# Kernel tuning notes

Measured on AMD Instinct MI355X. Metric: run time of the kernel, lower is better.

The kernel has to match this reference:

```python
import jax, jax.numpy as jnp
import numpy as np

DIM = 768
HEADS = 8
HEAD_DIM = DIM // HEADS
SCALE = DIM ** (-0.5)  # faithful: original scales by dimension**-0.5, not head_dim


def setup_inputs() -> dict:
    key = jax.random.key(0)
    k1, k2, k3 = jax.random.split(key, 3)
    B, N = 2, 4096
    x = jax.random.normal(k1, (B, N, DIM), dtype=jnp.float32)
    # qkv projection params (Linear(dim, 3*dim))
    W_qkv = jax.random.normal(k2, (DIM, 3 * DIM), dtype=jnp.float32) * (DIM ** -0.5)
    b_qkv = jax.random.normal(k3, (3 * DIM,), dtype=jnp.float32) * 0.01
    return {"x": x, "W_qkv": W_qkv, "b_qkv": b_qkv}


def reference(x, W_qkv, b_qkv):
    B, N, D = x.shape
    qkv = x @ W_qkv + b_qkv                       # (B, N, 3D)
    qkv = qkv.reshape(B, N, 3, HEADS, HEAD_DIM)
    q, k, v = jnp.moveaxis(qkv, 2, 0)             # each (B, N, H, dh)
    # (B, H, N, N) scores — explicit materialization as in the source
    scores = jnp.einsum('bnhd,bmhd->bhnm', q, k) * SCALE
    attn = jax.nn.softmax(scores, axis=-1)
    out = jnp.einsum('bhnm,bmhd->bnhd', attn, v)  # (B, N, H, dh)
    return out.reshape(B, N, D)
```

## Files before the change

### kernel.cpp

```cpp
#include <hip/hip_runtime.h>
#include <hip/hip_bf16.h>


typedef __attribute__((ext_vector_type(8)))  short    bf16x8;
typedef __attribute__((ext_vector_type(4)))  float    floatx4;
typedef __attribute__((ext_vector_type(16))) float    floatx16;
typedef __attribute__((ext_vector_type(8)))  unsigned short us8;
typedef __attribute__((ext_vector_type(4)))  unsigned short us4;

#define HEADS 8
#define DH 96
#define NSEQ 4096
#define DIM 768
#define SCALE2_F (0.03608439182435161f * 1.4426950408889634f)

__device__ __forceinline__ unsigned short f2bf(float f) {
    union { float f; unsigned u; } v; v.f = f;
    unsigned r = v.u + 0x7fffu + ((v.u >> 16) & 1u);
    return (unsigned short)(r >> 16);
}

__device__ __forceinline__ unsigned pk2(float a, float b) {
    float2 t; t.x = a; t.y = b;
    __hip_bfloat162 r = __float22bfloat162_rn(t);
    return *(unsigned*)&r;
}

__device__ __forceinline__ bf16x8 mk_pfrag(float c0, float c1, float c2, float c3,
                                           float c4, float c5, float c6, float c7, int hB) {
    unsigned pl0 = pk2(c0, c1), pl1 = pk2(c2, c3);
    unsigned pu0 = pk2(c4, c5), pu1 = pk2(c6, c7);
    unsigned s0 = hB ? pl0 : pu0, s1 = hB ? pl1 : pu1;
    unsigned r0 = (unsigned)__shfl_xor((int)s0, 32);
    unsigned r1 = (unsigned)__shfl_xor((int)s1, 32);
    union { unsigned u[4]; bf16x8 v; } f;
    f.u[0] = hB ? r0 : pl0;
    f.u[1] = hB ? r1 : pl1;
    f.u[2] = hB ? pu0 : r0;
    f.u[3] = hB ? pu1 : r1;
    return f.v;
}

__global__ __launch_bounds__(256) void cvt_x(const float* __restrict__ x, unsigned short* __restrict__ xb) {
    int i = blockIdx.x * 256 + threadIdx.x;
    float4 v = ((const float4*)x)[i];
    us4 o; o.x = f2bf(v.x); o.y = f2bf(v.y); o.z = f2bf(v.z); o.w = f2bf(v.w);
    ((us4*)xb)[i] = o;
}

__global__ __launch_bounds__(256) void cvt_w(const float* __restrict__ w, unsigned short* __restrict__ wt) {
    __shared__ unsigned short sm[64][33];
    int c0 = blockIdx.x * 32, k0 = blockIdx.y * 64;
    int t = threadIdx.x;
    int cl = t & 31, kl0 = t >> 5;
    for (int i = 0; i < 8; ++i) {
        int kl = kl0 + i * 8;
        sm[kl][cl] = f2bf(w[(k0 + kl) * 2304 + c0 + cl]);
    }
    __syncthreads();
    int kl2 = t & 63, cl0 = t >> 6;
    for (int i = 0; i < 8; ++i) {
        int cl2 = cl0 + i * 4;
        wt[(c0 + cl2) * 768 + k0 + kl2] = sm[kl2][cl2];
    }
}

__global__ __launch_bounds__(256) void gemm_qkv(const unsigned short* __restrict__ xb,
                                                const unsigned short* __restrict__ wt,
                                                const float* __restrict__ bias,
                                                unsigned short* __restrict__ qb,
                                                unsigned short* __restrict__ kb,
                                                unsigned short* __restrict__ vt) {
    __shared__ unsigned short As[128 * 72];
    __shared__ unsigned short Bs[128 * 72];
    const int tid = threadIdx.x;
    const int lane = tid & 63, wv = tid >> 6;
    const int n15 = lane & 15, quad = lane >> 4;
    const int m0 = blockIdx.y * 128, c0 = blockIdx.x * 128;
    const int mw = (wv >> 1) * 64, nw = (wv & 1) * 64;
    floatx4 acc[4][4] = {};

    for (int kt = 0; kt < 12; ++kt) {
        for (int i = 0; i < 4; ++i) {
            int g = i * 256 + tid;
            int row = g >> 3, gc = g & 7;
            *(us8*)&As[row * 72 + gc * 8] = *(const us8*)&xb[(m0 + row) * 768 + kt * 64 + gc * 8];
            *(us8*)&Bs[row * 72 + gc * 8] = *(const us8*)&wt[(c0 + row) * 768 + kt * 64 + gc * 8];
        }
        __syncthreads();
        for (int ks = 0; ks < 2; ++ks) {
            bf16x8 af[4], bfr[4];
            for (int mt = 0; mt < 4; ++mt)
                af[mt] = *(const bf16x8*)&As[(mw + mt * 16 + n15) * 72 + ks * 32 + quad * 8];
            for (int nt = 0; nt < 4; ++nt)
                bfr[nt] = *(const bf16x8*)&Bs[(nw + nt * 16 + n15) * 72 + ks * 32 + quad * 8];
            for (int mt = 0; mt < 4; ++mt)
                for (int nt = 0; nt < 4; ++nt)
                    acc[mt][nt] = __builtin_amdgcn_mfma_f32_16x16x32_bf16(af[mt], bfr[nt], acc[mt][nt], 0, 0, 0);
        }
        __syncthreads();
    }
    for (int nt = 0; nt < 4; ++nt) {
        int c = c0 + nw + nt * 16 + n15;
        float bv = bias[c];
        int which = c / 768, rem = c % 768;
        int h = rem / 96, d = rem % 96;
        for (int mt = 0; mt < 4; ++mt) {
            for (int r = 0; r < 4; ++r) {
                int m = m0 + mw + mt * 16 + quad * 4 + r;
                int b = m >> 12, n = m & 4095;
                float val = acc[mt][nt][r] + bv;
                int bh = b * HEADS + h;
                if (which == 0)      qb[(bh * NSEQ + n) * DH + d] = f2bf(val * SCALE2_F);
                else if (which == 1) kb[(bh * NSEQ + n) * DH + d] = f2bf(val);
                else                 vt[(bh * DH + d) * NSEQ + n] = f2bf(val);
            }
        }
    }
}

__global__ __launch_bounds__(128, 1) void flash(const unsigned short* __restrict__ qb,
                                                const unsigned short* __restrict__ kb,
                                                const unsigned short* __restrict__ vt,
                                                float* __restrict__ out) {
    __shared__ unsigned short sm[28672];
    __shared__ float l_all[128];

    const int tid = threadIdx.x;
    const int lane = tid & 63, wv = tid >> 6;
    const int l31 = lane & 31, h = lane >> 5;
    const int x7 = l31 & 7;
    const int id = blockIdx.x;
    const int bh = id & 15;
    const int q0 = (id >> 4) * 128 + wv * 64;

    const unsigned short* kgb = kb + (size_t)bh * NSEQ * DH;
    const unsigned short* vgb = vt + (size_t)bh * DH * NSEQ;

    bf16x8 qf[2][6];
#pragma unroll
    for (int qt = 0; qt < 2; ++qt) {
        const unsigned short* qrow = qb + (size_t)(bh * NSEQ + q0 + qt * 32 + l31) * DH;
#pragma unroll
        for (int ks = 0; ks < 6; ++ks)
            qf[qt][ks] = *(const bf16x8*)&qrow[ks * 16 + h * 8];
    }

    int kofs[2][6];
#pragma unroll
    for (int kt = 0; kt < 2; ++kt)
#pragma unroll
        for (int ks = 0; ks < 6; ++ks) {
            int b = 2 * ks + h;
            int bs = (b < 8) ? (b ^ x7) : (8 + ((b - 8) ^ x7));
            kofs[kt][ks] = (kt * 32 + l31) * 128 + bs * 8;
        }
    int vofs[3][4];
#pragma unroll
    for (int dt = 0; dt < 3; ++dt)
#pragma unroll
        for (int s = 0; s < 4; ++s)
            vofs[dt][s] = (dt * 32 + l31) * 64 + ((2 * s + h) ^ x7) * 8;

    int goffk[6], goffv[6], wofk[6], wofv[6];
#pragma unroll
    for (int i = 0; i < 6; ++i) {
        int tb = i * 128 + tid;
        int r = tb / 12, bb = tb % 12;
        goffk[i] = r * 96 + bb * 8;
        int bs = (bb < 8) ? (bb ^ (r & 7)) : (8 + ((bb - 8) ^ (r & 7)));
        wofk[i] = r * 128 + bs * 8;
        int d = tb >> 3, b2 = tb & 7;
        goffv[i] = d * 4096 + b2 * 8;
        wofv[i] = d * 64 + ((b2 ^ (d & 7))) * 8;
    }

    us8 kr[6], vr[6];
    const unsigned short* kpf = kgb;
    const unsigned short* vpf = vgb;
#pragma unroll
    for (int i = 0; i < 6; ++i) { kr[i] = *(const us8*)&kpf[goffk[i]]; vr[i] = *(const us8*)&vpf[goffv[i]]; }
    kpf += 6144; vpf += 64;
#pragma unroll
    for (int i = 0; i < 6; ++i) { *(us8*)&sm[wofk[i]] = kr[i]; *(us8*)&sm[16384 + wofv[i]] = vr[i]; }
#pragma unroll
    for (int i = 0; i < 6; ++i) { kr[i] = *(const us8*)&kpf[goffk[i]]; vr[i] = *(const us8*)&vpf[goffv[i]]; }
    kpf += 6144; vpf += 64;
    __syncthreads();

    floatx16 stA[2][2] = {}, stB[2][2] = {};
#pragma unroll
    for (int ks = 0; ks < 6; ++ks)
#pragma unroll
        for (int kt = 0; kt < 2; ++kt) {
            bf16x8 ak = *(const bf16x8*)&sm[kofs[kt][ks]];
            stA[kt][0] = __builtin_amdgcn_mfma_f32_32x32x16_bf16(ak, qf[0][ks], stA[kt][0], 0, 0, 0);
            stA[kt][1] = __builtin_amdgcn_mfma_f32_32x32x16_bf16(ak, qf[1][ks], stA[kt][1], 0, 0, 0);
        }

    floatx16 o[2][3] = {};
    float lsum[2] = {0.f, 0.f};

    auto body = [&](int kv, floatx16 (&cur)[2][2], floatx16 (&nxt)[2][2]) {
        const int nb = (kv + 1) & 1, cb = kv & 1;
        if (kv < 63) {
            unsigned short* Kd = sm + nb * 8192;
            unsigned short* Vd = sm + 16384 + nb * 6144;
#pragma unroll
            for (int i = 0; i < 6; ++i) { *(us8*)&Kd[wofk[i]] = kr[i]; *(us8*)&Vd[wofv[i]] = vr[i]; }
            if (kv < 62) {
#pragma unroll
                for (int i = 0; i < 6; ++i) { kr[i] = *(const us8*)&kpf[goffk[i]]; vr[i] = *(const us8*)&vpf[goffv[i]]; }
                kpf += 6144; vpf += 64;
            }
        }
        __syncthreads();

        const unsigned short* Kn = sm + nb * 8192;
        const unsigned short* Vc = sm + 16384 + cb * 6144;

        if (kv < 63) {
#pragma unroll
            for (int ks = 0; ks < 6; ++ks)
#pragma unroll
                for (int kt = 0; kt < 2; ++kt) {
                    bf16x8 ak = *(const bf16x8*)&Kn[kofs[kt][ks]];
                    nxt[kt][0] = __builtin_amdgcn_mfma_f32_32x32x16_bf16(ak, qf[0][ks], nxt[kt][0], 0, 0, 0);
                    nxt[kt][1] = __builtin_amdgcn_mfma_f32_32x32x16_bf16(ak, qf[1][ks], nxt[kt][1], 0, 0, 0);
                }
        }

#pragma unroll
        for (int kt = 0; kt < 2; ++kt)
#pragma unroll
            for (int qt = 0; qt < 2; ++qt)
#pragma unroll
                for (int rg = 0; rg < 16; ++rg) {
                    float p = __builtin_amdgcn_exp2f(cur[kt][qt][rg]);
                    cur[kt][qt][rg] = p;
                    lsum[qt] += p;
                }
        bf16x8 pf[2][4];
#pragma unroll
        for (int qt = 0; qt < 2; ++qt) {
            pf[qt][0] = mk_pfrag(cur[0][qt][0], cur[0][qt][1], cur[0][qt][2], cur[0][qt][3],
                                 cur[0][qt][4], cur[0][qt][5], cur[0][qt][6], cur[0][qt][7], h);
            pf[qt][1] = mk_pfrag(cur[0][qt][8], cur[0][qt][9], cur[0][qt][10], cur[0][qt][11],
                                 cur[0][qt][12], cur[0][qt][13], cur[0][qt][14], cur[0][qt][15], h);
            pf[qt][2] = mk_pfrag(cur[1][qt][0], cur[1][qt][1], cur[1][qt][2], cur[1][qt][3],
                                 cur[1][qt][4], cur[1][qt][5], cur[1][qt][6], cur[1][qt][7], h);
            pf[qt][3] = mk_pfrag(cur[1][qt][8], cur[1][qt][9], cur[1][qt][10], cur[1][qt][11],
                                 cur[1][qt][12], cur[1][qt][13], cur[1][qt][14], cur[1][qt][15], h);
        }
#pragma unroll
        for (int kt = 0; kt < 2; ++kt)
#pragma unroll
            for (int qt = 0; qt < 2; ++qt)
                cur[kt][qt] = (floatx16)(0.f);

#pragma unroll
        for (int s = 0; s < 4; ++s)
#pragma unroll
            for (int dt = 0; dt < 3; ++dt) {
                bf16x8 bv = *(const bf16x8*)&Vc[vofs[dt][s]];
                o[0][dt] = __builtin_amdgcn_mfma_f32_32x32x16_bf16(pf[0][s], bv, o[0][dt], 0, 0, 0);
                o[1][dt] = __builtin_amdgcn_mfma_f32_32x32x16_bf16(pf[1][s], bv, o[1][dt], 0, 0, 0);
            }

        __syncthreads();
    };

    for (int kv = 0; kv < 64; kv += 2) {
        body(kv, stA, stB);
        body(kv + 1, stB, stA);
    }

#pragma unroll
    for (int qt = 0; qt < 2; ++qt) {
        lsum[qt] += __shfl_xor(lsum[qt], 32);
        if (h == 0) l_all[wv * 64 + qt * 32 + l31] = lsum[qt];
    }
    __syncthreads();

    const int b = bh >> 3, hd = bh & 7;
#pragma unroll
    for (int qt = 0; qt < 2; ++qt)
#pragma unroll
        for (int rg = 0; rg < 16; ++rg) {
            int row = (rg & 3) + 8 * (rg >> 2) + 4 * h;
            float inv = 1.0f / l_all[wv * 64 + qt * 32 + row];
            int q = q0 + qt * 32 + row;
            float* op = out + (size_t)(b * NSEQ + q) * DIM + hd * DH;
#pragma unroll
            for (int dt = 0; dt < 3; ++dt)
                op[dt * 32 + l31] = o[qt][dt][rg] * inv;
        }
}

extern "C" void kernel_launch(void* const* d_in, const int* in_sizes, int n_in,
                              void* d_out, int out_size, void* d_ws, size_t ws_size,
                              hipStream_t stream) {
    const float* x    = (const float*)d_in[0];
    const float* W    = (const float*)d_in[1];
    const float* bias = (const float*)d_in[2];
    float* out = (float*)d_out;

    char* ws = (char*)d_ws;
    unsigned short* xb = (unsigned short*)(ws);
    unsigned short* wt = (unsigned short*)(ws + 12582912);
    unsigned short* qb = (unsigned short*)(ws + 16121856);
    unsigned short* kb = (unsigned short*)(ws + 28704768);
    unsigned short* vt = (unsigned short*)(ws + 41287680);

    cvt_x<<<6144, 256, 0, stream>>>(x, xb);
    cvt_w<<<dim3(72, 12), 256, 0, stream>>>(W, wt);
    gemm_qkv<<<dim3(18, 64), 256, 0, stream>>>(xb, wt, bias, qb, kb, vt);
    flash<<<512, 128, 0, stream>>>(qb, kb, vt, out);
}
```

Baseline: 279.4 us.

## Use four waves per flash block with 32 query rows each

The flash kernel now runs 256 threads per block, and each wave owns 32 query rows instead of 64. The block still covers 128 queries, so K/V tiles in shared memory are shared by four waves and each thread loads half as many K/V chunks. This cuts per-thread register use (accumulators, Q fragments, prefetch buffers) so launch bounds can request two blocks per CU, aiming for more latency hiding. In exchange each K tile fragment read from LDS feeds fewer MFMAs, which raises LDS traffic per unit of compute.

```diff
diff --git a/kernel.cpp b/kernel.cpp
--- a/kernel.cpp
+++ b/kernel.cpp
@@ -119,7 +119,7 @@
     }
 }
 
-__global__ __launch_bounds__(128, 1) void flash(const unsigned short* __restrict__ qb,
+__global__ __launch_bounds__(256, 2) void flash(const unsigned short* __restrict__ qb,
                                                 const unsigned short* __restrict__ kb,
                                                 const unsigned short* __restrict__ vt,
                                                 float* __restrict__ out) {
@@ -132,18 +132,17 @@
     const int x7 = l31 & 7;
     const int id = blockIdx.x;
     const int bh = id & 15;
-    const int q0 = (id >> 4) * 128 + wv * 64;
+    const int q0 = (id >> 4) * 128 + wv * 32;
 
     const unsigned short* kgb = kb + (size_t)bh * NSEQ * DH;
     const unsigned short* vgb = vt + (size_t)bh * DH * NSEQ;
 
-    bf16x8 qf[2][6];
-#pragma unroll
-    for (int qt = 0; qt < 2; ++qt) {
-        const unsigned short* qrow = qb + (size_t)(bh * NSEQ + q0 + qt * 32 + l31) * DH;
+    bf16x8 qf[6];
+    {
+        const unsigned short* qrow = qb + (size_t)(bh * NSEQ + q0 + l31) * DH;
 #pragma unroll
         for (int ks = 0; ks < 6; ++ks)
-            qf[qt][ks] = *(const bf16x8*)&qrow[ks * 16 + h * 8];
+            qf[ks] = *(const bf16x8*)&qrow[ks * 16 + h * 8];
     }
 
     int kofs[2][6];
@@ -162,10 +161,10 @@
         for (int s = 0; s < 4; ++s)
             vofs[dt][s] = (dt * 32 + l31) * 64 + ((2 * s + h) ^ x7) * 8;
 
-    int goffk[6], goffv[6], wofk[6], wofv[6];
-#pragma unroll
-    for (int i = 0; i < 6; ++i) {
-        int tb = i * 128 + tid;
+    int goffk[3], goffv[3], wofk[3], wofv[3];
+#pragma unroll
+    for (int i = 0; i < 3; ++i) {
+        int tb = i * 256 + tid;
         int r = tb / 12, bb = tb % 12;
         goffk[i] = r * 96 + bb * 8;
         int bs = (bb < 8) ? (bb ^ (r & 7)) : (8 + ((bb - 8) ^ (r & 7)));
@@ -175,42 +174,41 @@
         wofv[i] = d * 64 + ((b2 ^ (d & 7))) * 8;
     }
 
-    us8 kr[6], vr[6];
+    us8 kr[3], vr[3];
     const unsigned short* kpf = kgb;
     const unsigned short* vpf = vgb;
 #pragma unroll
-    for (int i = 0; i < 6; ++i) { kr[i] = *(const us8*)&kpf[goffk[i]]; vr[i] = *(const us8*)&vpf[goffv[i]]; }
+    for (int i = 0; i < 3; ++i) { kr[i] = *(const us8*)&kpf[goffk[i]]; vr[i] = *(const us8*)&vpf[goffv[i]]; }
     kpf += 6144; vpf += 64;
 #pragma unroll
-    for (int i = 0; i < 6; ++i) { *(us8*)&sm[wofk[i]] = kr[i]; *(us8*)&sm[16384 + wofv[i]] = vr[i]; }
-#pragma unroll
-    for (int i = 0; i < 6; ++i) { kr[i] = *(const us8*)&kpf[goffk[i]]; vr[i] = *(const us8*)&vpf[goffv[i]]; }
+    for (int i = 0; i < 3; ++i) { *(us8*)&sm[wofk[i]] = kr[i]; *(us8*)&sm[16384 + wofv[i]] = vr[i]; }
+#pragma unroll
+    for (int i = 0; i < 3; ++i) { kr[i] = *(const us8*)&kpf[goffk[i]]; vr[i] = *(const us8*)&vpf[goffv[i]]; }
     kpf += 6144; vpf += 64;
     __syncthreads();
 
-    floatx16 stA[2][2] = {}, stB[2][2] = {};
+    floatx16 stA[2] = {}, stB[2] = {};
 #pragma unroll
     for (int ks = 0; ks < 6; ++ks)
 #pragma unroll
         for (int kt = 0; kt < 2; ++kt) {
             bf16x8 ak = *(const bf16x8*)&sm[kofs[kt][ks]];
-            stA[kt][0] = __builtin_amdgcn_mfma_f32_32x32x16_bf16(ak, qf[0][ks], stA[kt][0], 0, 0, 0);
-            stA[kt][1] = __builtin_amdgcn_mfma_f32_32x32x16_bf16(ak, qf[1][ks], stA[kt][1], 0, 0, 0);
-        }
-
-    floatx16 o[2][3] = {};
-    float lsum[2] = {0.f, 0.f};
-
-    auto body = [&](int kv, floatx16 (&cur)[2][2], floatx16 (&nxt)[2][2]) {
+            stA[kt] = __builtin_amdgcn_mfma_f32_32x32x16_bf16(ak, qf[ks], stA[kt], 0, 0, 0);
+        }
+
+    floatx16 o[3] = {};
+    float lsum = 0.f;
+
+    auto body = [&](int kv, floatx16 (&cur)[2], floatx16 (&nxt)[2]) {
         const int nb = (kv + 1) & 1, cb = kv & 1;
         if (kv < 63) {
             unsigned short* Kd = sm + nb * 8192;
             unsigned short* Vd = sm + 16384 + nb * 6144;
 #pragma unroll
-            for (int i = 0; i < 6; ++i) { *(us8*)&Kd[wofk[i]] = kr[i]; *(us8*)&Vd[wofv[i]] = vr[i]; }
+            for (int i = 0; i < 3; ++i) { *(us8*)&Kd[wofk[i]] = kr[i]; *(us8*)&Vd[wofv[i]] = vr[i]; }
             if (kv < 62) {
 #pragma unroll
-                for (int i = 0; i < 6; ++i) { kr[i] = *(const us8*)&kpf[goffk[i]]; vr[i] = *(const us8*)&vpf[goffv[i]]; }
+                for (int i = 0; i < 3; ++i) { kr[i] = *(const us8*)&kpf[goffk[i]]; vr[i] = *(const us8*)&vpf[goffv[i]]; }
                 kpf += 6144; vpf += 64;
             }
         }
@@ -225,46 +223,37 @@
 #pragma unroll
                 for (int kt = 0; kt < 2; ++kt) {
                     bf16x8 ak = *(const bf16x8*)&Kn[kofs[kt][ks]];
-                    nxt[kt][0] = __builtin_amdgcn_mfma_f32_32x32x16_bf16(ak, qf[0][ks], nxt[kt][0], 0, 0, 0);
-                    nxt[kt][1] = __builtin_amdgcn_mfma_f32_32x32x16_bf16(ak, qf[1][ks], nxt[kt][1], 0, 0, 0);
+                    nxt[kt] = __builtin_amdgcn_mfma_f32_32x32x16_bf16(ak, qf[ks], nxt[kt], 0, 0, 0);
                 }
         }
 
 #pragma unroll
         for (int kt = 0; kt < 2; ++kt)
 #pragma unroll
-            for (int qt = 0; qt < 2; ++qt)
-#pragma unroll
-                for (int rg = 0; rg < 16; ++rg) {
-                    float p = __builtin_amdgcn_exp2f(cur[kt][qt][rg]);
-                    cur[kt][qt][rg] = p;
-                    lsum[qt] += p;
-                }
-        bf16x8 pf[2][4];
-#pragma unroll
-        for (int qt = 0; qt < 2; ++qt) {
-            pf[qt][0] = mk_pfrag(cur[0][qt][0], cur[0][qt][1], cur[0][qt][2], cur[0][qt][3],
-                                 cur[0][qt][4], cur[0][qt][5], cur[0][qt][6], cur[0][qt][7], h);
-            pf[qt][1] = mk_pfrag(cur[0][qt][8], cur[0][qt][9], cur[0][qt][10], cur[0][qt][11],
-                                 cur[0][qt][12], cur[0][qt][13], cur[0][qt][14], cur[0][qt][15], h);
-            pf[qt][2] = mk_pfrag(cur[1][qt][0], cur[1][qt][1], cur[1][qt][2], cur[1][qt][3],
-                                 cur[1][qt][4], cur[1][qt][5], cur[1][qt][6], cur[1][qt][7], h);
-            pf[qt][3] = mk_pfrag(cur[1][qt][8], cur[1][qt][9], cur[1][qt][10], cur[1][qt][11],
-                                 cur[1][qt][12], cur[1][qt][13], cur[1][qt][14], cur[1][qt][15], h);
-        }
+            for (int rg = 0; rg < 16; ++rg) {
+                float p = __builtin_amdgcn_exp2f(cur[kt][rg]);
+                cur[kt][rg] = p;
+                lsum += p;
+            }
+        bf16x8 pf[4];
+        pf[0] = mk_pfrag(cur[0][0], cur[0][1], cur[0][2], cur[0][3],
+                         cur[0][4], cur[0][5], cur[0][6], cur[0][7], h);
+        pf[1] = mk_pfrag(cur[0][8], cur[0][9], cur[0][10], cur[0][11],
+                         cur[0][12], cur[0][13], cur[0][14], cur[0][15], h);
+        pf[2] = mk_pfrag(cur[1][0], cur[1][1], cur[1][2], cur[1][3],
+                         cur[1][4], cur[1][5], cur[1][6], cur[1][7], h);
+        pf[3] = mk_pfrag(cur[1][8], cur[1][9], cur[1][10], cur[1][11],
+                         cur[1][12], cur[1][13], cur[1][14], cur[1][15], h);
 #pragma unroll
         for (int kt = 0; kt < 2; ++kt)
-#pragma unroll
-            for (int qt = 0; qt < 2; ++qt)
-                cur[kt][qt] = (floatx16)(0.f);
+            cur[kt] = (floatx16)(0.f);
 
 #pragma unroll
         for (int s = 0; s < 4; ++s)
 #pragma unroll
             for (int dt = 0; dt < 3; ++dt) {
                 bf16x8 bv = *(const bf16x8*)&Vc[vofs[dt][s]];
-                o[0][dt] = __builtin_amdgcn_mfma_f32_32x32x16_bf16(pf[0][s], bv, o[0][dt], 0, 0, 0);
-                o[1][dt] = __builtin_amdgcn_mfma_f32_32x32x16_bf16(pf[1][s], bv, o[1][dt], 0, 0, 0);
+                o[dt] = __builtin_amdgcn_mfma_f32_32x32x16_bf16(pf[s], bv, o[dt], 0, 0, 0);
             }
 
         __syncthreads();
@@ -275,26 +264,21 @@
         body(kv + 1, stB, stA);
     }
 
-#pragma unroll
-    for (int qt = 0; qt < 2; ++qt) {
-        lsum[qt] += __shfl_xor(lsum[qt], 32);
-        if (h == 0) l_all[wv * 64 + qt * 32 + l31] = lsum[qt];
-    }
+    lsum += __shfl_xor(lsum, 32);
+    if (h == 0) l_all[wv * 32 + l31] = lsum;
     __syncthreads();
 
     const int b = bh >> 3, hd = bh & 7;
 #pragma unroll
-    for (int qt = 0; qt < 2; ++qt)
-#pragma unroll
-        for (int rg = 0; rg < 16; ++rg) {
-            int row = (rg & 3) + 8 * (rg >> 2) + 4 * h;
-            float inv = 1.0f / l_all[wv * 64 + qt * 32 + row];
-            int q = q0 + qt * 32 + row;
-            float* op = out + (size_t)(b * NSEQ + q) * DIM + hd * DH;
-#pragma unroll
-            for (int dt = 0; dt < 3; ++dt)
-                op[dt * 32 + l31] = o[qt][dt][rg] * inv;
-        }
+    for (int rg = 0; rg < 16; ++rg) {
+        int row = (rg & 3) + 8 * (rg >> 2) + 4 * h;
+        float inv = 1.0f / l_all[wv * 32 + row];
+        int q = q0 + row;
+        float* op = out + (size_t)(b * NSEQ + q) * DIM + hd * DH;
+#pragma unroll
+        for (int dt = 0; dt < 3; ++dt)
+            op[dt * 32 + l31] = o[dt][rg] * inv;
+    }
 }
 
 extern "C" void kernel_launch(void* const* d_in, const int* in_sizes, int n_in,
@@ -315,5 +299,5 @@
     cvt_x<<<6144, 256, 0, stream>>>(x, xb);
     cvt_w<<<dim3(72, 12), 256, 0, stream>>>(W, wt);
     gemm_qkv<<<dim3(18, 64), 256, 0, stream>>>(xb, wt, bias, qb, kb, vt);
-    flash<<<512, 128, 0, stream>>>(qb, kb, vt, out);
-}
+    flash<<<512, 256, 0, stream>>>(qb, kb, vt, out);
+}
```

Result: faster. 259.1 us (-7.2%).
